# Optimization experiments

Hardware: AMD Instinct MI355X
Metric: run time of the kernel (lower is better)

## Reference

```python
import jax, jax.numpy as jnp
import numpy as np

N = 65536          # query points (rays * samples per chunk)
C = 2048           # num_codes in code cloud
K = 16             # knn neighbors
CD = 64            # code_dim
IN_XYZ = 63        # positional-encoded xyz channels
IN_DIR = 27        # positional-encoded dir channels
W = 128            # decoder width (D=4, skips=[2])
DIST_SCALE = 2.0


def setup_inputs() -> dict:
    key = jax.random.key(0)
    ks = jax.random.split(key, 16)

    def glorot(k, shape):
        return jax.random.normal(k, shape, jnp.float32) / np.float32(np.sqrt(shape[0]))

    in_x = CD + IN_XYZ  # decoder in_channels_xyz = 127
    inp = {
        "indices": jnp.zeros((1,), jnp.int32),
        "query_points": jax.random.uniform(ks[0], (N, 3), jnp.float32),
        "xyzdir_embedded": jax.random.normal(ks[1], (N, IN_XYZ + IN_DIR), jnp.float32),
        "codes_position": jax.random.uniform(ks[2], (1, C, 3), jnp.float32),
        "codes": jax.random.normal(ks[3], (1, C, CD), jnp.float32) * 0.01,
        # decoder params
        "W0": glorot(ks[4], (in_x, W)), "b0": jnp.zeros((W,), jnp.float32),
        "W1": glorot(ks[5], (W, W)), "b1": jnp.zeros((W,), jnp.float32),
        "W2": glorot(ks[6], (W + in_x, W)), "b2": jnp.zeros((W,), jnp.float32),  # skip layer i=2
        "W3": glorot(ks[7], (W, W)), "b3": jnp.zeros((W,), jnp.float32),
        "Wf": glorot(ks[8], (W, W)), "bf": jnp.zeros((W,), jnp.float32),          # xyz_encoding_final
        "Wd": glorot(ks[9], (W + IN_DIR, W // 2)), "bd": jnp.zeros((W // 2,), jnp.float32),
        "Ws": glorot(ks[10], (W, 1)), "bs": jnp.zeros((1,), jnp.float32),
        "Wr": glorot(ks[11], (W // 2, 3)), "br": jnp.zeros((3,), jnp.float32),
    }
    return inp


def _knn_idx(q, c, k):
    # brute-force L2 knn (faiss replacement); indices only, no grad (torch no_grad)
    q = jax.lax.stop_gradient(q)
    c = jax.lax.stop_gradient(c)
    d2 = (jnp.sum(q * q, -1, keepdims=True)
          - 2.0 * q @ c.T
          + jnp.sum(c * c, -1))  # (N, C)
    _, idx = jax.lax.top_k(-d2, k)  # (N, K) nearest
    return idx


def reference(indices, query_points, xyzdir_embedded, codes_position, codes,
              W0, b0, W1, b1, W2, b2, W3, b3, Wf, bf, Wd, bd, Ws, bs, Wr, br):
    # --- CodeCloud.query ---
    cp = codes_position[indices][0]      # (C, 3)
    cc = codes[indices][0]               # (C, CD)
    idx = _knn_idx(query_points, cp, K)  # (N, K)
    neigh_pos = cp[idx]                  # (N, K, 3)
    sq = jnp.sum((query_points[:, None, :] - neigh_pos) ** 2, -1) + 1e-16  # (N, K)
    w = 1.0 / jnp.sqrt(sq) ** DIST_SCALE
    w = w / jnp.sum(w, -1, keepdims=True)
    neigh_codes = cc[idx]                # (N, K, CD)
    query_codes = jnp.einsum("nk,nkd->nd", w, neigh_codes)  # (N, CD)

    # --- IM_Decoder (D=4, W=128, skips=[2]) ---
    x = jnp.concatenate([query_codes, xyzdir_embedded], -1)  # (N, 127+27)
    in_x = CD + IN_XYZ
    input_xyz, input_dir = x[:, :in_x], x[:, in_x:]
    h = jax.nn.relu(input_xyz @ W0 + b0)
    h = jax.nn.relu(h @ W1 + b1)
    h = jax.nn.relu(jnp.concatenate([input_xyz, h], -1) @ W2 + b2)  # skip at i=2
    h = jax.nn.relu(h @ W3 + b3)
    sigma = h @ Ws + bs                       # (N, 1)
    final = h @ Wf + bf                       # (N, W)
    d = jax.nn.relu(jnp.concatenate([final, input_dir], -1) @ Wd + bd)
    rgb = d @ Wr + br                         # (N, 3)
    return jnp.concatenate([rgb, sigma], -1)  # (N, 4)
```

## Files before the change

### kernel.cpp

```cpp
#include <hip/hip_runtime.h>

#define N_Q   65536
#define N_C   2048
#define KNN_K 16
#define CDIM  64
#define SLCAP 128
#define KINF  0x7FFFFFFF
#define WSZ   108544

typedef _Float16 half_t;
typedef float v4f __attribute__((ext_vector_type(4)));
typedef half_t v8h __attribute__((ext_vector_type(8)));

#define ASTRIDE 136
#define DSTRIDE 40

__device__ __forceinline__ int dppx(int v, int j){
  if (j == 1) return __builtin_amdgcn_mov_dpp(v, 0xB1,  0xF, 0xF, true);
  if (j == 2) return __builtin_amdgcn_mov_dpp(v, 0x4E,  0xF, 0xF, true);
  if (j == 8) return __builtin_amdgcn_mov_dpp(v, 0x128, 0xF, 0xF, true);
  return __shfl_xor(v, j, 64);
}
__device__ __forceinline__ float dppxf(float v, int j){
  return __int_as_float(dppx(__float_as_int(v), j));
}

__global__ void wtrans_kernel(const float* W0, const float* W1, const float* W2,
                              const float* W3, const float* Wf, const float* Wd,
                              const int* indices, const float* cpos,
                              half_t* wt, float4* cpos4){
  int idx = blockIdx.x * 256 + threadIdx.x;
  if (idx >= 110592) return;
  if (idx >= WSZ){
    int i = idx - WSZ;
    const float* cp = cpos + (size_t)indices[0] * N_C * 3;
    float x = cp[i*3 + 0], y = cp[i*3 + 1], z = cp[i*3 + 2];
    cpos4[i] = make_float4(x, y, z, fmaf(x, x, fmaf(y, y, fmaf(z, z, 4.0f))));
    return;
  }
  int base, nt, mode;
  const float* src = W1;
  if (idx < 16384){ base = 0; nt = 8; mode = 1; }
  else if (idx < 32768){ base = 16384; nt = 8; mode = 0; src = W1; }
  else if (idx < 65536){ base = 32768; nt = 8; mode = 2; }
  else if (idx < 81920){ base = 65536; nt = 8; mode = 0; src = W3; }
  else if (idx < 98304){ base = 81920; nt = 8; mode = 0; src = Wf; }
  else { base = 98304; nt = 4; mode = 3; }
  int i = idx - base;
  int tile = i >> 9, e = i & 511;
  int lane = e >> 3, j = e & 7;
  int k0idx = tile / nt, tcol = tile - k0idx*nt;
  int n = tcol*16 + (lane & 15);
  int k = k0idx*32 + ((lane >> 4) << 3) + j;
  float val;
  if (mode == 0)      val = src[k*128 + n];
  else if (mode == 1) val = (k < 127) ? W0[k*128 + n] : 0.f;
  else if (mode == 2) val = (k == 127) ? 0.f
                           : ((k < 127) ? W2[k*128 + n] : W2[(k-1)*128 + n]);
  else                val = (k < 155) ? Wd[k*64 + n] : 0.f;
  wt[idx] = (half_t)val;
}

__global__ __launch_bounds__(512, 6) void knn_kernel(const int* indices,
    const float* qpts, const float4* cpos4, const float* codes,
    const float* xyzdir, half_t* Ain, half_t* Din){
  __shared__ float4 lp[N_C];
  __shared__ int    sl[8*SLCAP];
  int tid = threadIdx.x;
  int lane = tid & 63, wave = tid >> 6;
  int l = lane & 15;
  const float* cc = codes + (size_t)indices[0] * N_C * CDIM;

  for (int c = tid; c < N_C; c += 512) lp[c] = cpos4[c];
  __syncthreads();

  int q = blockIdx.x * 8 + wave;
  float qx = qpts[q*3 + 0];
  float qy = qpts[q*3 + 1];
  float qz = qpts[q*3 + 2];
  float nqx = -2.0f*qx, nqy = -2.0f*qy, nqz = -2.0f*qz;

  int p[32];
#pragma unroll
  for (int j = 0; j < 32; j++){
    int c = j*64 + lane;
    float4 P = lp[c];
    float s = fmaf(P.x, nqx, fmaf(P.y, nqy, fmaf(P.z, nqz, P.w)));
    int pv = (__float_as_int(s) & 0xFFFFF800) | c;
    asm("" : "+v"(pv));
    p[j] = pv;
  }

  int lm = p[0];
#pragma unroll
  for (int j = 1; j < 32; j++) lm = min(lm, p[j]);

  int v = lm;
#pragma unroll
  for (int k = 2; k <= 16; k <<= 1){
#pragma unroll
    for (int j = k >> 1; j > 0; j >>= 1){
      int o = dppx(v, j);
      bool dirDesc = (l & k) != 0;
      bool lower   = (l & j) == 0;
      int mn = min(v, o), mx = max(v, o);
      v = (lower != dirDesc) ? mn : mx;
    }
  }
  int t0 = __shfl(v, 3, 64),  t1 = __shfl(v, 19, 64);
  int t2 = __shfl(v, 35, 64), t3 = __shfl(v, 51, 64);
  int tau = max(max(t0, t1), max(t2, t3));

  int* slw = &sl[wave * SLCAP];
  int n = 0;
#pragma unroll
  for (int j = 0; j < 32; j++){
    bool c = (p[j] <= tau);
    unsigned long long m = __ballot(c);
    if (m){
      if (n <= 64){
        if (c){
          int mb = __builtin_amdgcn_mbcnt_hi((unsigned)(m >> 32),
                   __builtin_amdgcn_mbcnt_lo((unsigned)m, 0));
          slw[n + mb] = p[j];
        }
      }
      n += (int)__popcll(m);
    }
  }
  __builtin_amdgcn_wave_barrier();

  int keep;
  if (n >= KNN_K && n <= 64){
    int x = (lane < n) ? slw[lane] : KINF;
#pragma unroll
    for (int k = 2; k <= 16; k <<= 1){
#pragma unroll
      for (int j = k >> 1; j > 0; j >>= 1){
        int o = dppx(x, j);
        bool dirDesc = (l & k) != 0;
        bool lower   = (l & j) == 0;
        int mn = min(x, o), mx = max(x, o);
        x = (lower != dirDesc) ? mn : mx;
      }
    }
    x = min(x, __shfl_xor(x, 31, 64));
#pragma unroll
    for (int j = 8; j > 0; j >>= 1){
      int o = dppx(x, j);
      bool lower = (l & j) == 0;
      int mn = min(x, o), mx = max(x, o);
      x = lower ? mn : mx;
    }
    x = min(x, __shfl_xor(x, 63, 64));
    keep = x;
  } else {
    keep = KINF;
#pragma unroll 1
    for (int rr = 0; rr < KNN_K; rr++){
      int lmf = p[0];
#pragma unroll
      for (int j = 1; j < 32; j++) lmf = min(lmf, p[j]);
      int gm = lmf;
#pragma unroll
      for (int off2 = 1; off2 < 64; off2 <<= 1)
        gm = min(gm, __shfl_xor(gm, off2, 64));
      if (lane == rr) keep = gm;
#pragma unroll
      for (int j = 0; j < 32; j++) p[j] = (p[j] == gm) ? KINF : p[j];
    }
  }

  int ci = keep & 0x7FF;
  float4 P = lp[ci];
  float dx = qx - P.x, dy = qy - P.y, dz = qz - P.z;
  float d2 = fmaf(dz, dz, fmaf(dy, dy, dx*dx));
  float w = 1.0f / (d2 + 1e-16f);
  float wm = (lane < KNN_K) ? w : 0.0f;
  wm += dppxf(wm, 1);
  wm += dppxf(wm, 2);
  wm += __shfl_xor(wm, 4, 64);
  wm += dppxf(wm, 8);
  float wn = w / wm;

  float acc = 0.f;
#pragma unroll
  for (int i = 0; i < KNN_K; i++){
    int   cb = __shfl(ci, i, 64);
    float wb = __shfl(wn, i, 64);
    acc = fmaf(wb, cc[cb*CDIM + lane], acc);
  }
  size_t arow = (size_t)q * ASTRIDE;
  Ain[arow + lane] = (half_t)acc;

  float xv = (lane < 63) ? xyzdir[(size_t)q*90 + lane] : 0.f;
  Ain[arow + 64 + lane] = (half_t)xv;
  if (lane < 8) Ain[arow + 128 + lane] = (half_t)0.f;
  if (lane < 40){
    float dv = (lane < 27) ? xyzdir[(size_t)q*90 + 63 + lane] : 0.f;
    Din[(size_t)q*DSTRIDE + lane] = (half_t)dv;
  }
}

template<int NCH, int NT>
__device__ inline void mfma_pl(const half_t* act, int astride, int rowbase,
                               const half_t* wlayer, int nt, int ktbase,
                               int tcolbase, v4f acc[2][NT], int lane){
  v8h breg[NCH*NT];
#pragma unroll
  for (int c = 0; c < NCH; c++){
#pragma unroll
    for (int t = 0; t < NT; t++){
      const half_t* bp = wlayer +
          ((size_t)(((ktbase + c)*nt + tcolbase + t) << 9) + (lane << 3));
      breg[c*NT + t] = *(const v8h*)bp;
    }
  }
  int m = lane & 15, quad = lane >> 4;
#pragma unroll
  for (int c = 0; c < NCH; c++){
    v8h a0 = *(const v8h*)&act[(rowbase + m)*astride + c*32 + quad*8];
    v8h a1 = *(const v8h*)&act[(rowbase + 16 + m)*astride + c*32 + quad*8];
#pragma unroll
    for (int t = 0; t < NT; t++){
      acc[0][t] = __builtin_amdgcn_mfma_f32_16x16x32_f16(a0, breg[c*NT + t], acc[0][t], 0, 0, 0);
      acc[1][t] = __builtin_amdgcn_mfma_f32_16x16x32_f16(a1, breg[c*NT + t], acc[1][t], 0, 0, 0);
    }
  }
}

template<int NT>
__device__ inline void epilogue64(v4f acc[2][NT], half_t* outb, int rowbase,
                                  int colbase, const float* bias, bool relu,
                                  int lane){
  int n = lane & 15, quad = lane >> 4;
#pragma unroll
  for (int t = 0; t < NT; t++){
    int col = colbase + t*16 + n;
    float bv = bias[col];
#pragma unroll
    for (int g = 0; g < 2; g++){
#pragma unroll
      for (int r = 0; r < 4; r++){
        float v = acc[g][t][r] + bv;
        if (relu) v = fmaxf(v, 0.f);
        outb[(rowbase + g*16 + quad*4 + r)*ASTRIDE + col] = (half_t)v;
      }
    }
  }
}

__global__ __launch_bounds__(512, 6) void mlp_mfma(
    const half_t* Ain, const half_t* Din, const half_t* wt,
    const float* b0, const float* b1, const float* b2, const float* b3,
    const float* bfb, const float* bdb,
    const float* Wsb, const float* bsb, const float* Wrb, const float* brb,
    float* out){
  __shared__ __align__(16) half_t Abuf[64*ASTRIDE];
  __shared__ __align__(16) half_t Pbuf[64*ASTRIDE];
  __shared__ __align__(16) half_t Qbuf[64*ASTRIDE];

  int tid = threadIdx.x, lane = tid & 63, wave = tid >> 6;
  int qbase = blockIdx.x * 64;

  for (int i = tid; i < 64*17; i += 512){
    int r = i / 17, c8 = i - r*17;
    *(uint4*)&Abuf[r*ASTRIDE + (c8 << 3)] =
        *(const uint4*)&Ain[(size_t)(qbase + r)*ASTRIDE + (c8 << 3)];
  }
  __syncthreads();

  int rowbase  = (wave >> 2) * 32;
  int colq     = wave & 3;
  int colbase  = colq * 32;
  int tcolbase = colq * 2;
  v4f acc[2][2];
  v4f accd[2][1];

  const half_t* wt0 = wt;
  const half_t* wt1 = wt + 16384;
  const half_t* wt2 = wt + 32768;
  const half_t* wt3 = wt + 65536;
  const half_t* wtf = wt + 81920;
  const half_t* wtd = wt + 98304;

#define ZACC22() { for (int g_ = 0; g_ < 2; g_++) for (int t_ = 0; t_ < 2; t_++) \
                   for (int e_ = 0; e_ < 4; e_++) acc[g_][t_][e_] = 0.f; }

  ZACC22();
  mfma_pl<4,2>(Abuf, ASTRIDE, rowbase, wt0, 8, 0, tcolbase, acc, lane);
  epilogue64<2>(acc, Pbuf, rowbase, colbase, b0, true, lane);
  __syncthreads();

  ZACC22();
  mfma_pl<4,2>(Pbuf, ASTRIDE, rowbase, wt1, 8, 0, tcolbase, acc, lane);
  epilogue64<2>(acc, Qbuf, rowbase, colbase, b1, true, lane);
  __syncthreads();

  ZACC22();
  mfma_pl<4,2>(Abuf, ASTRIDE, rowbase, wt2, 8, 0, tcolbase, acc, lane);
  mfma_pl<4,2>(Qbuf, ASTRIDE, rowbase, wt2, 8, 4, tcolbase, acc, lane);
  epilogue64<2>(acc, Pbuf, rowbase, colbase, b2, true, lane);
  __syncthreads();

  ZACC22();
  mfma_pl<4,2>(Pbuf, ASTRIDE, rowbase, wt3, 8, 0, tcolbase, acc, lane);
  epilogue64<2>(acc, Abuf, rowbase, colbase, b3, true, lane);
  __syncthreads();

  ZACC22();
  mfma_pl<4,2>(Abuf, ASTRIDE, rowbase, wtf, 8, 0, tcolbase, acc, lane);
  epilogue64<2>(acc, Pbuf, rowbase, colbase, bfb, false, lane);
  __syncthreads();

#pragma unroll
  for (int g_ = 0; g_ < 2; g_++)
#pragma unroll
    for (int e_ = 0; e_ < 4; e_++) accd[g_][0][e_] = 0.f;
  mfma_pl<4,1>(Pbuf, ASTRIDE, rowbase, wtd, 4, 0, colq, accd, lane);
  mfma_pl<1,1>(Din + (size_t)qbase*DSTRIDE, DSTRIDE, rowbase, wtd, 4, 4, colq,
               accd, lane);
  epilogue64<1>(accd, Qbuf, rowbase, colq * 16, bdb, true, lane);
  __syncthreads();

  {
    int q = tid >> 3, part = tid & 7;
    float s = 0.f;
#pragma unroll
    for (int k = 0; k < 16; k++){
      int kk = part*16 + k;
      s = fmaf((float)Abuf[q*ASTRIDE + kk], Wsb[kk], s);
    }
    s += __shfl_xor(s, 1, 64); s += __shfl_xor(s, 2, 64); s += __shfl_xor(s, 4, 64);

    float r3[3];
#pragma unroll
    for (int c2 = 0; c2 < 3; c2++){
      float rv = 0.f;
#pragma unroll
      for (int k = 0; k < 8; k++){
        int kk = part*8 + k;
        rv = fmaf((float)Qbuf[q*ASTRIDE + kk], Wrb[kk*3 + c2], rv);
      }
      rv += __shfl_xor(rv, 1, 64); rv += __shfl_xor(rv, 2, 64); rv += __shfl_xor(rv, 4, 64);
      r3[c2] = rv;
    }
    if (part == 0){
      size_t ob = ((size_t)(qbase + q)) * 4;
      out[ob + 0] = r3[0] + brb[0];
      out[ob + 1] = r3[1] + brb[1];
      out[ob + 2] = r3[2] + brb[2];
      out[ob + 3] = s + bsb[0];
    }
  }
}

extern "C" void kernel_launch(void* const* d_in, const int* in_sizes, int n_in,
                              void* d_out, int out_size, void* d_ws, size_t ws_size,
                              hipStream_t stream){
  (void)in_sizes; (void)n_in; (void)out_size; (void)ws_size;

  const int*   indices = (const int*)d_in[0];
  const float* qpts    = (const float*)d_in[1];
  const float* xyzdir  = (const float*)d_in[2];
  const float* cpos    = (const float*)d_in[3];
  const float* codes   = (const float*)d_in[4];
  const float* W0 = (const float*)d_in[5];
  const float* b0 = (const float*)d_in[6];
  const float* W1 = (const float*)d_in[7];
  const float* b1 = (const float*)d_in[8];
  const float* W2 = (const float*)d_in[9];
  const float* b2 = (const float*)d_in[10];
  const float* W3 = (const float*)d_in[11];
  const float* b3 = (const float*)d_in[12];
  const float* Wf = (const float*)d_in[13];
  const float* bf = (const float*)d_in[14];
  const float* Wd = (const float*)d_in[15];
  const float* bd = (const float*)d_in[16];
  const float* Ws = (const float*)d_in[17];
  const float* bs = (const float*)d_in[18];
  const float* Wr = (const float*)d_in[19];
  const float* br = (const float*)d_in[20];

  half_t* Ain   = (half_t*)d_ws;
  half_t* Din   = (half_t*)((char*)d_ws + 17825792);
  half_t* wt    = (half_t*)((char*)d_ws + 17825792 + 5242880);
  float4* cpos4 = (float4*)((char*)d_ws + 17825792 + 5242880 + 217088);

  wtrans_kernel<<<(110592 + 255)/256, 256, 0, stream>>>(W0, W1, W2, W3, Wf, Wd,
                                                        indices, cpos, wt, cpos4);
  knn_kernel<<<N_Q/8, 512, 0, stream>>>(indices, qpts, cpos4, codes, xyzdir,
                                        Ain, Din);
  mlp_mfma<<<N_Q/64, 512, 0, stream>>>(Ain, Din, wt,
                                       b0, b1, b2, b3, bf, bd, Ws, bs, Wr, br,
                                       (float*)d_out);
}
```

Before: 205.8 us.

## Restructure MLP kernel so each wave owns 16 rows independently without block barriers

The decoder MLP kernel now gives each wave a private 16-row tile with its own LDS buffers and computes all output columns per wave. This removes every __syncthreads between layers, and the sigma and rgb heads are reduced with cross-quad shuffles and written out with a vectorized float4 store. The trade-off is that each wave now loads the full weight matrix from global/L2 instead of a quarter of it, which raises weight traffic per row. It also keeps 8 accumulator tiles live, which raises register pressure.

```diff
diff --git a/kernel.cpp b/kernel.cpp
--- a/kernel.cpp
+++ b/kernel.cpp
@@ -202,80 +202,71 @@
   }
 }
 
-template<int NCH, int NT>
-__device__ inline void mfma_pl(const half_t* act, int astride, int rowbase,
-                               const half_t* wlayer, int nt, int ktbase,
-                               int tcolbase, v4f acc[2][NT], int lane){
-  v8h breg[NCH*NT];
-#pragma unroll
-  for (int c = 0; c < NCH; c++){
+template<int KC, int NT>
+__device__ __forceinline__ void wave_layer(const half_t* inb, int istride,
+                                           const half_t* wlayer, int nt_total,
+                                           int ktbase, v4f acc[NT], int lane){
+  int m = lane & 15, quad = lane >> 4;
+  v8h areg[KC];
+#pragma unroll
+  for (int c = 0; c < KC; c++)
+    areg[c] = *(const v8h*)&inb[m*istride + (c << 5) + (quad << 3)];
+#pragma unroll
+  for (int c = 0; c < KC; c++){
 #pragma unroll
     for (int t = 0; t < NT; t++){
       const half_t* bp = wlayer +
-          ((size_t)(((ktbase + c)*nt + tcolbase + t) << 9) + (lane << 3));
-      breg[c*NT + t] = *(const v8h*)bp;
-    }
-  }
-  int m = lane & 15, quad = lane >> 4;
-#pragma unroll
-  for (int c = 0; c < NCH; c++){
-    v8h a0 = *(const v8h*)&act[(rowbase + m)*astride + c*32 + quad*8];
-    v8h a1 = *(const v8h*)&act[(rowbase + 16 + m)*astride + c*32 + quad*8];
-#pragma unroll
-    for (int t = 0; t < NT; t++){
-      acc[0][t] = __builtin_amdgcn_mfma_f32_16x16x32_f16(a0, breg[c*NT + t], acc[0][t], 0, 0, 0);
-      acc[1][t] = __builtin_amdgcn_mfma_f32_16x16x32_f16(a1, breg[c*NT + t], acc[1][t], 0, 0, 0);
+          ((size_t)(((ktbase + c)*nt_total + t) << 9) + (lane << 3));
+      v8h b = *(const v8h*)bp;
+      acc[t] = __builtin_amdgcn_mfma_f32_16x16x32_f16(areg[c], b, acc[t], 0, 0, 0);
     }
   }
 }
 
 template<int NT>
-__device__ inline void epilogue64(v4f acc[2][NT], half_t* outb, int rowbase,
-                                  int colbase, const float* bias, bool relu,
-                                  int lane){
-  int n = lane & 15, quad = lane >> 4;
+__device__ __forceinline__ void wave_epi(v4f acc[NT], half_t* outb, int ostride,
+                                         const float* bias, bool relu, int lane){
+  int m16 = lane & 15, quad = lane >> 4;
 #pragma unroll
   for (int t = 0; t < NT; t++){
-    int col = colbase + t*16 + n;
+    int col = t*16 + m16;
     float bv = bias[col];
 #pragma unroll
-    for (int g = 0; g < 2; g++){
-#pragma unroll
-      for (int r = 0; r < 4; r++){
-        float v = acc[g][t][r] + bv;
-        if (relu) v = fmaxf(v, 0.f);
-        outb[(rowbase + g*16 + quad*4 + r)*ASTRIDE + col] = (half_t)v;
-      }
-    }
-  }
-}
-
-__global__ __launch_bounds__(512, 6) void mlp_mfma(
+    for (int r = 0; r < 4; r++){
+      float v = acc[t][r] + bv;
+      if (relu) v = fmaxf(v, 0.f);
+      outb[(quad*4 + r)*ostride + col] = (half_t)v;
+    }
+  }
+}
+
+__global__ __launch_bounds__(256, 4) void mlp_mfma(
     const half_t* Ain, const half_t* Din, const half_t* wt,
     const float* b0, const float* b1, const float* b2, const float* b3,
     const float* bfb, const float* bdb,
     const float* Wsb, const float* bsb, const float* Wrb, const float* brb,
     float* out){
-  __shared__ __align__(16) half_t Abuf[64*ASTRIDE];
-  __shared__ __align__(16) half_t Pbuf[64*ASTRIDE];
-  __shared__ __align__(16) half_t Qbuf[64*ASTRIDE];
+  __shared__ __align__(16) half_t bufA[4][16*ASTRIDE];
+  __shared__ __align__(16) half_t bufB[4][16*ASTRIDE];
+  __shared__ __align__(16) half_t bufD[4][16*DSTRIDE];
 
   int tid = threadIdx.x, lane = tid & 63, wave = tid >> 6;
-  int qbase = blockIdx.x * 64;
-
-  for (int i = tid; i < 64*17; i += 512){
+  int qbase = (blockIdx.x * 4 + wave) * 16;
+
+  half_t* A = bufA[wave];
+  half_t* B = bufB[wave];
+  half_t* D = bufD[wave];
+
+  for (int i = lane; i < 16*17; i += 64){
     int r = i / 17, c8 = i - r*17;
-    *(uint4*)&Abuf[r*ASTRIDE + (c8 << 3)] =
+    *(uint4*)&A[r*ASTRIDE + (c8 << 3)] =
         *(const uint4*)&Ain[(size_t)(qbase + r)*ASTRIDE + (c8 << 3)];
   }
-  __syncthreads();
-
-  int rowbase  = (wave >> 2) * 32;
-  int colq     = wave & 3;
-  int colbase  = colq * 32;
-  int tcolbase = colq * 2;
-  v4f acc[2][2];
-  v4f accd[2][1];
+  for (int i = lane; i < 16*5; i += 64){
+    int r = i / 5, c8 = i - r*5;
+    *(uint4*)&D[r*DSTRIDE + (c8 << 3)] =
+        *(const uint4*)&Din[(size_t)(qbase + r)*DSTRIDE + (c8 << 3)];
+  }
 
   const half_t* wt0 = wt;
   const half_t* wt1 = wt + 16384;
@@ -284,73 +275,80 @@
   const half_t* wtf = wt + 81920;
   const half_t* wtd = wt + 98304;
 
-#define ZACC22() { for (int g_ = 0; g_ < 2; g_++) for (int t_ = 0; t_ < 2; t_++) \
-                   for (int e_ = 0; e_ < 4; e_++) acc[g_][t_][e_] = 0.f; }
-
-  ZACC22();
-  mfma_pl<4,2>(Abuf, ASTRIDE, rowbase, wt0, 8, 0, tcolbase, acc, lane);
-  epilogue64<2>(acc, Pbuf, rowbase, colbase, b0, true, lane);
-  __syncthreads();
-
-  ZACC22();
-  mfma_pl<4,2>(Pbuf, ASTRIDE, rowbase, wt1, 8, 0, tcolbase, acc, lane);
-  epilogue64<2>(acc, Qbuf, rowbase, colbase, b1, true, lane);
-  __syncthreads();
-
-  ZACC22();
-  mfma_pl<4,2>(Abuf, ASTRIDE, rowbase, wt2, 8, 0, tcolbase, acc, lane);
-  mfma_pl<4,2>(Qbuf, ASTRIDE, rowbase, wt2, 8, 4, tcolbase, acc, lane);
-  epilogue64<2>(acc, Pbuf, rowbase, colbase, b2, true, lane);
-  __syncthreads();
-
-  ZACC22();
-  mfma_pl<4,2>(Pbuf, ASTRIDE, rowbase, wt3, 8, 0, tcolbase, acc, lane);
-  epilogue64<2>(acc, Abuf, rowbase, colbase, b3, true, lane);
-  __syncthreads();
-
-  ZACC22();
-  mfma_pl<4,2>(Abuf, ASTRIDE, rowbase, wtf, 8, 0, tcolbase, acc, lane);
-  epilogue64<2>(acc, Pbuf, rowbase, colbase, bfb, false, lane);
-  __syncthreads();
-
-#pragma unroll
-  for (int g_ = 0; g_ < 2; g_++)
-#pragma unroll
-    for (int e_ = 0; e_ < 4; e_++) accd[g_][0][e_] = 0.f;
-  mfma_pl<4,1>(Pbuf, ASTRIDE, rowbase, wtd, 4, 0, colq, accd, lane);
-  mfma_pl<1,1>(Din + (size_t)qbase*DSTRIDE, DSTRIDE, rowbase, wtd, 4, 4, colq,
-               accd, lane);
-  epilogue64<1>(accd, Qbuf, rowbase, colq * 16, bdb, true, lane);
-  __syncthreads();
-
+  v4f acc[8];
+#define ZACC8() { _Pragma("unroll") for (int t_ = 0; t_ < 8; t_++) \
+                  _Pragma("unroll") for (int e_ = 0; e_ < 4; e_++) acc[t_][e_] = 0.f; }
+
+  ZACC8();
+  wave_layer<4,8>(A, ASTRIDE, wt0, 8, 0, acc, lane);
+  wave_epi<8>(acc, B, ASTRIDE, b0, true, lane);
+
+  ZACC8();
+  wave_layer<4,8>(B, ASTRIDE, wt1, 8, 0, acc, lane);
+  wave_epi<8>(acc, B, ASTRIDE, b1, true, lane);
+
+  ZACC8();
+  wave_layer<4,8>(A, ASTRIDE, wt2, 8, 0, acc, lane);
+  wave_layer<4,8>(B, ASTRIDE, wt2, 8, 4, acc, lane);
+  wave_epi<8>(acc, B, ASTRIDE, b2, true, lane);
+
+  ZACC8();
+  wave_layer<4,8>(B, ASTRIDE, wt3, 8, 0, acc, lane);
+  wave_epi<8>(acc, B, ASTRIDE, b3, true, lane);
+
+  ZACC8();
+  wave_layer<4,8>(B, ASTRIDE, wtf, 8, 0, acc, lane);
+  wave_epi<8>(acc, A, ASTRIDE, bfb, false, lane);
+
+  int m16 = lane & 15, quad = lane >> 4;
+  float sig;
   {
-    int q = tid >> 3, part = tid & 7;
     float s = 0.f;
 #pragma unroll
-    for (int k = 0; k < 16; k++){
-      int kk = part*16 + k;
-      s = fmaf((float)Abuf[q*ASTRIDE + kk], Wsb[kk], s);
-    }
-    s += __shfl_xor(s, 1, 64); s += __shfl_xor(s, 2, 64); s += __shfl_xor(s, 4, 64);
-
-    float r3[3];
+    for (int i = 0; i < 4; i++){
+      v8h hv = *(const v8h*)&B[m16*ASTRIDE + quad*32 + i*8];
+      float4 w0 = *(const float4*)&Wsb[quad*32 + i*8];
+      float4 w1 = *(const float4*)&Wsb[quad*32 + i*8 + 4];
+      s = fmaf((float)hv[0], w0.x, s); s = fmaf((float)hv[1], w0.y, s);
+      s = fmaf((float)hv[2], w0.z, s); s = fmaf((float)hv[3], w0.w, s);
+      s = fmaf((float)hv[4], w1.x, s); s = fmaf((float)hv[5], w1.y, s);
+      s = fmaf((float)hv[6], w1.z, s); s = fmaf((float)hv[7], w1.w, s);
+    }
+    s += __shfl_xor(s, 16, 64);
+    s += __shfl_xor(s, 32, 64);
+    sig = s;
+  }
+
+  v4f accd[4];
+#pragma unroll
+  for (int t_ = 0; t_ < 4; t_++)
+#pragma unroll
+    for (int e_ = 0; e_ < 4; e_++) accd[t_][e_] = 0.f;
+  wave_layer<4,4>(A, ASTRIDE, wtd, 4, 0, accd, lane);
+  wave_layer<1,4>(D, DSTRIDE, wtd, 4, 4, accd, lane);
+  wave_epi<4>(accd, B, ASTRIDE, bdb, true, lane);
+
+  {
+    float r3[3] = {0.f, 0.f, 0.f};
+    v8h d0 = *(const v8h*)&B[m16*ASTRIDE + quad*16];
+    v8h d1 = *(const v8h*)&B[m16*ASTRIDE + quad*16 + 8];
 #pragma unroll
     for (int c2 = 0; c2 < 3; c2++){
       float rv = 0.f;
 #pragma unroll
       for (int k = 0; k < 8; k++){
-        int kk = part*8 + k;
-        rv = fmaf((float)Qbuf[q*ASTRIDE + kk], Wrb[kk*3 + c2], rv);
+        rv = fmaf((float)d0[k], Wrb[(quad*16 + k)*3 + c2], rv);
+        rv = fmaf((float)d1[k], Wrb[(quad*16 + 8 + k)*3 + c2], rv);
       }
-      rv += __shfl_xor(rv, 1, 64); rv += __shfl_xor(rv, 2, 64); rv += __shfl_xor(rv, 4, 64);
+      rv += __shfl_xor(rv, 16, 64);
+      rv += __shfl_xor(rv, 32, 64);
       r3[c2] = rv;
     }
-    if (part == 0){
-      size_t ob = ((size_t)(qbase + q)) * 4;
-      out[ob + 0] = r3[0] + brb[0];
-      out[ob + 1] = r3[1] + brb[1];
-      out[ob + 2] = r3[2] + brb[2];
-      out[ob + 3] = s + bsb[0];
+    if (quad == 0){
+      size_t ob = ((size_t)(qbase + m16)) * 4;
+      float4 o4 = make_float4(r3[0] + brb[0], r3[1] + brb[1],
+                              r3[2] + brb[2], sig + bsb[0]);
+      *(float4*)&out[ob] = o4;
     }
   }
 }
@@ -391,7 +389,7 @@
                                                         indices, cpos, wt, cpos4);
   knn_kernel<<<N_Q/8, 512, 0, stream>>>(indices, qpts, cpos4, codes, xyzdir,
                                         Ain, Din);
-  mlp_mfma<<<N_Q/64, 512, 0, stream>>>(Ain, Din, wt,
+  mlp_mfma<<<N_Q/64, 256, 0, stream>>>(Ain, Din, wt,
                                        b0, b1, b2, b3, bf, bd, Ws, bs, Wr, br,
                                        (float*)d_out);
 }
```

Result: slower. 239.5 us (+16.4%).

## Process two queries per wave in KNN and recompute distances instead of caching

Applied to the files above, without the earlier changes.

Each wave now handles two query points, sharing every LDS load of a code position between both distance computations and interleaving the two bitonic sorts and ballot passes to expose ILP. The 32-entry per-lane register array is dropped: distances are recomputed in the threshold-compaction pass and again in a slower fallback, which lowers register pressure and allows launch bounds of 8 waves per SIMD. The cost is extra FMA work per candidate and a serial per-round rescan of all candidates when the fallback path triggers.

```diff
diff --git a/kernel.cpp b/kernel.cpp
--- a/kernel.cpp
+++ b/kernel.cpp
@@ -61,116 +61,70 @@
   wt[idx] = (half_t)val;
 }
 
-__global__ __launch_bounds__(512, 6) void knn_kernel(const int* indices,
-    const float* qpts, const float4* cpos4, const float* codes,
-    const float* xyzdir, half_t* Ain, half_t* Din){
-  __shared__ float4 lp[N_C];
-  __shared__ int    sl[8*SLCAP];
-  int tid = threadIdx.x;
-  int lane = tid & 63, wave = tid >> 6;
-  int l = lane & 15;
-  const float* cc = codes + (size_t)indices[0] * N_C * CDIM;
-
-  for (int c = tid; c < N_C; c += 512) lp[c] = cpos4[c];
-  __syncthreads();
-
-  int q = blockIdx.x * 8 + wave;
-  float qx = qpts[q*3 + 0];
-  float qy = qpts[q*3 + 1];
-  float qz = qpts[q*3 + 2];
-  float nqx = -2.0f*qx, nqy = -2.0f*qy, nqz = -2.0f*qz;
-
-  int p[32];
-#pragma unroll
-  for (int j = 0; j < 32; j++){
-    int c = j*64 + lane;
-    float4 P = lp[c];
-    float s = fmaf(P.x, nqx, fmaf(P.y, nqy, fmaf(P.z, nqz, P.w)));
-    int pv = (__float_as_int(s) & 0xFFFFF800) | c;
-    asm("" : "+v"(pv));
-    p[j] = pv;
-  }
-
-  int lm = p[0];
-#pragma unroll
-  for (int j = 1; j < 32; j++) lm = min(lm, p[j]);
-
-  int v = lm;
+__device__ __forceinline__ void sort16_dual(int& va, int& vb, int l){
 #pragma unroll
   for (int k = 2; k <= 16; k <<= 1){
 #pragma unroll
     for (int j = k >> 1; j > 0; j >>= 1){
-      int o = dppx(v, j);
+      int oa = dppx(va, j);
+      int ob = dppx(vb, j);
       bool dirDesc = (l & k) != 0;
       bool lower   = (l & j) == 0;
-      int mn = min(v, o), mx = max(v, o);
-      v = (lower != dirDesc) ? mn : mx;
-    }
-  }
-  int t0 = __shfl(v, 3, 64),  t1 = __shfl(v, 19, 64);
-  int t2 = __shfl(v, 35, 64), t3 = __shfl(v, 51, 64);
-  int tau = max(max(t0, t1), max(t2, t3));
-
-  int* slw = &sl[wave * SLCAP];
-  int n = 0;
-#pragma unroll
-  for (int j = 0; j < 32; j++){
-    bool c = (p[j] <= tau);
-    unsigned long long m = __ballot(c);
-    if (m){
-      if (n <= 64){
-        if (c){
-          int mb = __builtin_amdgcn_mbcnt_hi((unsigned)(m >> 32),
-                   __builtin_amdgcn_mbcnt_lo((unsigned)m, 0));
-          slw[n + mb] = p[j];
-        }
-      }
-      n += (int)__popcll(m);
-    }
-  }
-  __builtin_amdgcn_wave_barrier();
-
-  int keep;
-  if (n >= KNN_K && n <= 64){
-    int x = (lane < n) ? slw[lane] : KINF;
-#pragma unroll
-    for (int k = 2; k <= 16; k <<= 1){
-#pragma unroll
-      for (int j = k >> 1; j > 0; j >>= 1){
-        int o = dppx(x, j);
-        bool dirDesc = (l & k) != 0;
-        bool lower   = (l & j) == 0;
-        int mn = min(x, o), mx = max(x, o);
-        x = (lower != dirDesc) ? mn : mx;
-      }
-    }
-    x = min(x, __shfl_xor(x, 31, 64));
-#pragma unroll
-    for (int j = 8; j > 0; j >>= 1){
-      int o = dppx(x, j);
-      bool lower = (l & j) == 0;
-      int mn = min(x, o), mx = max(x, o);
-      x = lower ? mn : mx;
-    }
-    x = min(x, __shfl_xor(x, 63, 64));
-    keep = x;
-  } else {
-    keep = KINF;
+      int mna = min(va, oa), mxa = max(va, oa);
+      int mnb = min(vb, ob), mxb = max(vb, ob);
+      va = (lower != dirDesc) ? mna : mxa;
+      vb = (lower != dirDesc) ? mnb : mxb;
+    }
+  }
+}
+
+__device__ __forceinline__ void sel16_dual(int& xa, int& xb, int l){
+  sort16_dual(xa, xb, l);
+  xa = min(xa, __shfl_xor(xa, 31, 64));
+  xb = min(xb, __shfl_xor(xb, 31, 64));
+#pragma unroll
+  for (int j = 8; j > 0; j >>= 1){
+    int oa = dppx(xa, j), ob = dppx(xb, j);
+    bool lower = (l & j) == 0;
+    int mna = min(xa, oa), mxa = max(xa, oa);
+    int mnb = min(xb, ob), mxb = max(xb, ob);
+    xa = lower ? mna : mxa;
+    xb = lower ? mnb : mxb;
+  }
+  xa = min(xa, __shfl_xor(xa, 63, 64));
+  xb = min(xb, __shfl_xor(xb, 63, 64));
+}
+
+__device__ __forceinline__ int knn_fallback(const float4* lp, float nqx,
+                                            float nqy, float nqz, int lane){
+  unsigned used = 0u;
+  int keep = KINF;
 #pragma unroll 1
-    for (int rr = 0; rr < KNN_K; rr++){
-      int lmf = p[0];
-#pragma unroll
-      for (int j = 1; j < 32; j++) lmf = min(lmf, p[j]);
-      int gm = lmf;
-#pragma unroll
-      for (int off2 = 1; off2 < 64; off2 <<= 1)
-        gm = min(gm, __shfl_xor(gm, off2, 64));
-      if (lane == rr) keep = gm;
-#pragma unroll
-      for (int j = 0; j < 32; j++) p[j] = (p[j] == gm) ? KINF : p[j];
-    }
-  }
-
+  for (int rr = 0; rr < KNN_K; rr++){
+    int best = KINF;
+#pragma unroll 1
+    for (int j = 0; j < 32; j++){
+      int c = j*64 + lane;
+      float4 P = lp[c];
+      float s = fmaf(P.x, nqx, fmaf(P.y, nqy, fmaf(P.z, nqz, P.w)));
+      int pv = (__float_as_int(s) & 0xFFFFF800) | c;
+      pv = ((used >> j) & 1u) ? KINF : pv;
+      best = min(best, pv);
+    }
+    int gm = best;
+#pragma unroll
+    for (int off2 = 1; off2 < 64; off2 <<= 1)
+      gm = min(gm, __shfl_xor(gm, off2, 64));
+    if (lane == rr) keep = gm;
+    int gc = gm & 0x7FF;
+    if ((gc & 63) == lane) used |= (1u << (gc >> 6));
+  }
+  return keep;
+}
+
+__device__ __forceinline__ void knn_tail(int keep, const float4* lp,
+    float qx, float qy, float qz, const float* cc, const float* xyzdir,
+    half_t* Ain, half_t* Din, int q, int lane){
   int ci = keep & 0x7FF;
   float4 P = lp[ci];
   float dx = qx - P.x, dy = qy - P.y, dz = qz - P.z;
@@ -200,6 +154,87 @@
     float dv = (lane < 27) ? xyzdir[(size_t)q*90 + 63 + lane] : 0.f;
     Din[(size_t)q*DSTRIDE + lane] = (half_t)dv;
   }
+}
+
+__global__ __launch_bounds__(512, 8) void knn_kernel(const int* indices,
+    const float* qpts, const float4* cpos4, const float* codes,
+    const float* xyzdir, half_t* Ain, half_t* Din){
+  __shared__ float4 lp[N_C];
+  __shared__ int    sl[16*SLCAP];
+  int tid = threadIdx.x;
+  int lane = tid & 63, wave = tid >> 6;
+  int l = lane & 15;
+  const float* cc = codes + (size_t)indices[0] * N_C * CDIM;
+
+  for (int c = tid; c < N_C; c += 512) lp[c] = cpos4[c];
+  __syncthreads();
+
+  int qA = blockIdx.x * 16 + wave * 2;
+  int qB = qA + 1;
+  float qxA = qpts[qA*3 + 0], qyA = qpts[qA*3 + 1], qzA = qpts[qA*3 + 2];
+  float qxB = qpts[qB*3 + 0], qyB = qpts[qB*3 + 1], qzB = qpts[qB*3 + 2];
+  float nqxA = -2.0f*qxA, nqyA = -2.0f*qyA, nqzA = -2.0f*qzA;
+  float nqxB = -2.0f*qxB, nqyB = -2.0f*qyB, nqzB = -2.0f*qzB;
+
+  int minA = KINF, minB = KINF;
+#pragma unroll
+  for (int j = 0; j < 32; j++){
+    int c = j*64 + lane;
+    float4 P = lp[c];
+    float sA = fmaf(P.x, nqxA, fmaf(P.y, nqyA, fmaf(P.z, nqzA, P.w)));
+    float sB = fmaf(P.x, nqxB, fmaf(P.y, nqyB, fmaf(P.z, nqzB, P.w)));
+    minA = min(minA, (__float_as_int(sA) & 0xFFFFF800) | c);
+    minB = min(minB, (__float_as_int(sB) & 0xFFFFF800) | c);
+  }
+
+  int vA = minA, vB = minB;
+  sort16_dual(vA, vB, l);
+  int tauA = max(max(__shfl(vA, 3, 64), __shfl(vA, 19, 64)),
+                 max(__shfl(vA, 35, 64), __shfl(vA, 51, 64)));
+  int tauB = max(max(__shfl(vB, 3, 64), __shfl(vB, 19, 64)),
+                 max(__shfl(vB, 35, 64), __shfl(vB, 51, 64)));
+
+  int* slwA = &sl[(wave*2 + 0) * SLCAP];
+  int* slwB = &sl[(wave*2 + 1) * SLCAP];
+  int nA = 0, nB = 0;
+#pragma unroll
+  for (int j = 0; j < 32; j++){
+    int c = j*64 + lane;
+    float4 P = lp[c];
+    float sA = fmaf(P.x, nqxA, fmaf(P.y, nqyA, fmaf(P.z, nqzA, P.w)));
+    float sB = fmaf(P.x, nqxB, fmaf(P.y, nqyB, fmaf(P.z, nqzB, P.w)));
+    int pvA = (__float_as_int(sA) & 0xFFFFF800) | c;
+    int pvB = (__float_as_int(sB) & 0xFFFFF800) | c;
+
+    bool cA = (pvA <= tauA);
+    unsigned long long mA = __ballot(cA);
+    int mbA = __builtin_amdgcn_mbcnt_hi((unsigned)(mA >> 32),
+              __builtin_amdgcn_mbcnt_lo((unsigned)mA, 0));
+    if (cA && nA <= 64) slwA[nA + mbA] = pvA;
+    nA += (int)__popcll(mA);
+
+    bool cB = (pvB <= tauB);
+    unsigned long long mB = __ballot(cB);
+    int mbB = __builtin_amdgcn_mbcnt_hi((unsigned)(mB >> 32),
+              __builtin_amdgcn_mbcnt_lo((unsigned)mB, 0));
+    if (cB && nB <= 64) slwB[nB + mbB] = pvB;
+    nB += (int)__popcll(mB);
+  }
+  __builtin_amdgcn_wave_barrier();
+
+  bool okA = (nA >= KNN_K && nA <= 64);
+  bool okB = (nB >= KNN_K && nB <= 64);
+
+  int xA = (lane < nA) ? slwA[lane] : KINF;
+  int xB = (lane < nB) ? slwB[lane] : KINF;
+  sel16_dual(xA, xB, l);
+  int keepA = xA, keepB = xB;
+
+  if (!okA) keepA = knn_fallback(lp, nqxA, nqyA, nqzA, lane);
+  if (!okB) keepB = knn_fallback(lp, nqxB, nqyB, nqzB, lane);
+
+  knn_tail(keepA, lp, qxA, qyA, qzA, cc, xyzdir, Ain, Din, qA, lane);
+  knn_tail(keepB, lp, qxB, qyB, qzB, cc, xyzdir, Ain, Din, qB, lane);
 }
 
 template<int NCH, int NT>
@@ -389,8 +424,8 @@
 
   wtrans_kernel<<<(110592 + 255)/256, 256, 0, stream>>>(W0, W1, W2, W3, Wf, Wd,
                                                         indices, cpos, wt, cpos4);
-  knn_kernel<<<N_Q/8, 512, 0, stream>>>(indices, qpts, cpos4, codes, xyzdir,
-                                        Ain, Din);
+  knn_kernel<<<N_Q/16, 512, 0, stream>>>(indices, qpts, cpos4, codes, xyzdir,
+                                         Ain, Din);
   mlp_mfma<<<N_Q/64, 512, 0, stream>>>(Ain, Din, wt,
                                        b0, b1, b2, b3, bf, bd, Ws, bs, Wr, br,
                                        (float*)d_out);
```

After: 233.8 us. 1.14x slower.
